# Kernel optimization log

Hardware: AMD Instinct MI355X
Metric: run time of the kernel (lower is better)

Reference implementation:

```python
import jax, jax.numpy as jnp
import numpy as np

NEG = jnp.float32(-1e9)  # -inf surrogate, safe for logsumexp
EPS = 1e-7               # keras.backend.epsilon()


def _ctc_loss(y_true, y_pred):
    """Faithful K.ctc_batch_cost with full input/label lengths.

    y_true: [B, L] int labels in [0, C-2] (blank = C-1, TF convention)
    y_pred: [B, T, C] softmax probabilities
    returns: [B, 1] negative log-likelihood per sample
    """
    B, T, C = y_pred.shape
    L = y_true.shape[1]
    blank = C - 1
    S = 2 * L + 1  # extended label: blank-interleaved

    logp = jnp.log(y_pred + EPS)  # [B, T, C]

    # Extended label sequence [blank, l1, blank, l2, ..., lL, blank]
    ext = jnp.full((B, S), blank, dtype=jnp.int32).at[:, 1::2].set(
        y_true.astype(jnp.int32))  # [B, S]

    # Skip transition (s-2 -> s) allowed iff ext[s] != blank and ext[s] != ext[s-2]
    skip = jnp.concatenate(
        [jnp.zeros((B, 2), dtype=bool),
         (ext[:, 2:] != blank) & (ext[:, 2:] != ext[:, :-2])],
        axis=1)  # [B, S]

    # Gather lattice log-probs once: [B, T, S]
    lp = jnp.take_along_axis(logp, ext[:, None, :], axis=2)

    # alpha at t=0: only states 0 (blank) and 1 (first label) reachable
    alpha0 = jnp.full((B, S), NEG).at[:, 0].set(lp[:, 0, 0]).at[:, 1].set(lp[:, 0, 1])

    def step(alpha, lp_t):
        a1 = alpha                                                     # stay
        a2 = jnp.pad(alpha[:, :-1], ((0, 0), (1, 0)), constant_values=NEG)  # advance 1
        a3 = jnp.pad(alpha[:, :-2], ((0, 0), (2, 0)), constant_values=NEG)  # advance 2
        a3 = jnp.where(skip, a3, NEG)
        new = lp_t + jax.nn.logsumexp(jnp.stack([a1, a2, a3]), axis=0)
        return new, None

    lp_rest = jnp.transpose(lp[:, 1:, :], (1, 0, 2))  # [T-1, B, S]
    alphaT, _ = jax.lax.scan(step, alpha0, lp_rest)

    # Total log-prob ends in last blank or last label
    ll = jax.nn.logsumexp(alphaT[:, S - 2:S], axis=1)  # [B]
    return -ll[:, None]  # [B, 1], matches ctc_batch_cost's expand_dims


def setup_inputs() -> dict:
    key = jax.random.key(0)
    k1, k2 = jax.random.split(key)
    B, T, C, L = 512, 512, 128, 64
    logits = jax.random.normal(k1, (B, T, C), dtype=jnp.float32)
    y_pred = jax.nn.softmax(logits, axis=-1)  # ctc_batch_cost expects probs
    y_true = jax.random.randint(k2, (B, L), 0, C - 1)  # labels exclude blank C-1
    return {"y_true": y_true, "y_pred": y_pred}


def reference(y_true, y_pred):
    return _ctc_loss(y_true, y_pred)
```

## Files before the change

kernel.cpp:

```cpp
#include <hip/hip_runtime.h>


constexpr float EPSF = 1e-7f;
constexpr float LN2F = 0.6931471805599453f;

template<int CTRL>
__device__ __forceinline__ float dpp_mov(float x) {
    return __int_as_float(__builtin_amdgcn_update_dpp(
        0, __float_as_int(x), CTRL, 0xF, 0xF, true));
}

__global__ __launch_bounds__(64)
void ctc_fwd(const int* __restrict__ y_true,
             const float* __restrict__ y_pred,
             float* __restrict__ out)
{
    const int b    = blockIdx.x;
    const int lane = threadIdx.x;

    const float4* __restrict__ gsrc =
        (const float4*)(y_pred + (size_t)b * 512 * 128);

    __shared__ __align__(16) float lds[2 * 2048];

    const int   lab   = y_true[b * 64 + lane];
    const int   labp  = __shfl_up(lab, 1, 64);
    const float skipf = (lane > 0 && lab != labp) ? 1.0f : 0.0f;
    const bool  l0    = (lane == 0);

    float4 regs[3][8];

    auto issueLoads = [&](int chunk, int set) {
        #pragma unroll
        for (int k = 0; k < 8; ++k)
            regs[set][k] = gsrc[chunk * 512 + k * 64 + lane];
    };
    auto writeChunk = [&](int chunk, int set) {
        float* dst = &lds[(chunk & 1) * 2048];
        #pragma unroll
        for (int k = 0; k < 8; ++k)
            *(float4*)(dst + k * 256 + lane * 4) = regs[set][k];
    };

    float plr[4], pbr[4];
    auto issueRead = [&](int t) {
        int tn = t > 511 ? 511 : t;
        const float* rb = &lds[((tn >> 4) & 1) * 2048 + (tn & 15) * 128];
        plr[t & 3] = rb[lab];
        pbr[t & 3] = rb[127];
    };

    float aZ, aA, aB;
    int   shift = 0;
    float red   = 0.0f;

    auto consume = [&](int t, int j) {
        float pl = plr[j & 3] + EPSF;
        float pb = pbr[j & 3] + EPSF;
        float upA = dpp_mov<0x138>(aA);
        float upB = dpp_mov<0x138>(aB);
        upB = l0 ? aZ : upB;
        float ts = fmaf(skipf, upA, aA + upB);
        float nA = pl * ts;
        float nB = pb * (aB + aA);
        aZ *= pb;
        aA = nA; aB = nB;
        if ((j & 7) == 3) {
            float r = fmaxf(fmaxf(aA, aB), aZ);
            r = fmaxf(r, dpp_mov<0x111>(r));
            r = fmaxf(r, dpp_mov<0x112>(r));
            r = fmaxf(r, dpp_mov<0x114>(r));
            r = fmaxf(r, dpp_mov<0x118>(r));
            r = fmaxf(r, dpp_mov<0x142>(r));
            r = fmaxf(r, dpp_mov<0x143>(r));
            red = r;
        }
        if ((j & 7) == 7) {
            int mb = __builtin_amdgcn_readlane(__float_as_int(red), 63);
            int e  = (mb >> 23) & 0xff;
            int f  = 314 - e;
            f = f < 1 ? 1 : (f > 254 ? 254 : f);
            float scale = __int_as_float(f << 23);
            shift += f - 127;
            aA *= scale; aB *= scale; aZ *= scale;
        }
        issueRead(t + 4);
    };

    issueLoads(0, 0); issueLoads(1, 1); issueLoads(2, 2);
    writeChunk(0, 0);
    issueRead(0); issueRead(1); issueRead(2); issueRead(3);
    {
        float pb0 = pbr[0] + EPSF;
        float pl0 = plr[0] + EPSF;
        aZ = pb0;
        aA = l0 ? pl0 : 0.0f;
        aB = 0.0f;
    }
    issueRead(4);

    issueLoads(3, 0);
    writeChunk(1, 1);
    #pragma unroll
    for (int j = 1; j < 16; ++j) consume(j, j);

    for (int cb = 1; cb <= 28; cb += 3) {
        {
            int c = cb;
            if (c + 3 < 32) issueLoads(c + 3, 1);
            writeChunk(c + 1, 2);
            #pragma unroll
            for (int j = 0; j < 16; ++j) consume(16 * c + j, j);
        }
        {
            int c = cb + 1;
            if (c + 3 < 32) issueLoads(c + 3, 2);
            writeChunk(c + 1, 0);
            #pragma unroll
            for (int j = 0; j < 16; ++j) consume(16 * c + j, j);
        }
        {
            int c = cb + 2;
            if (c + 3 < 32) issueLoads(c + 3, 0);
            writeChunk(c + 1, 1);
            #pragma unroll
            for (int j = 0; j < 16; ++j) consume(16 * c + j, j);
        }
    }

    #pragma unroll
    for (int j = 0; j < 16; ++j) consume(16 * 31 + j, j);

    float s   = aA + aB;
    float ll2 = __builtin_amdgcn_logf(s);
    if (lane == 63) out[b] = ((float)shift - ll2) * LN2F;
}

extern "C" void kernel_launch(void* const* d_in, const int* in_sizes, int n_in,
                              void* d_out, int out_size, void* d_ws, size_t ws_size,
                              hipStream_t stream)
{
    const int*   y_true = (const int*)d_in[0];
    const float* y_pred = (const float*)d_in[1];
    float*       out    = (float*)d_out;

    const int B = out_size;
    ctc_fwd<<<dim3(B), dim3(64), 0, stream>>>(y_true, y_pred, out);
}
```

Baseline: 216.8 us.

## Stream probabilities directly into LDS via global_load_lds with 8-deep ring buffer

Replaces the register-staged triple-buffer (global load into VGPRs, then LDS store) with direct global-to-LDS async loads into an 8-chunk ring buffer, throttled by manual vmcnt waits. This is meant to free VGPRs, drop the LDS write instructions from the serial recurrence loop, and keep more loads in flight to hide latency. It raises LDS use to 64KB per block, which may limit occupancy, and correctness depends on the hand-encoded waitcnt values and the absence of barriers within a single wave.

```diff
diff --git a/kernel.cpp b/kernel.cpp
--- a/kernel.cpp
+++ b/kernel.cpp
@@ -10,6 +10,9 @@
         0, __float_as_int(x), CTRL, 0xF, 0xF, true));
 }
 
+#define WAITVM(n) __builtin_amdgcn_s_waitcnt( ((n) & 0xF) | ((((n) >> 4) & 0x3) << 14) \
+                                            | (0x7 << 4) | (0xF << 8) )
+
 __global__ __launch_bounds__(64)
 void ctc_fwd(const int* __restrict__ y_true,
              const float* __restrict__ y_pred,
@@ -18,36 +21,32 @@
     const int b    = blockIdx.x;
     const int lane = threadIdx.x;
 
+    __shared__ __align__(16) float lds[8 * 2048];
+
     const float4* __restrict__ gsrc =
         (const float4*)(y_pred + (size_t)b * 512 * 128);
-
-    __shared__ __align__(16) float lds[2 * 2048];
 
     const int   lab   = y_true[b * 64 + lane];
     const int   labp  = __shfl_up(lab, 1, 64);
     const float skipf = (lane > 0 && lab != labp) ? 1.0f : 0.0f;
     const bool  l0    = (lane == 0);
 
-    float4 regs[3][8];
-
-    auto issueLoads = [&](int chunk, int set) {
+    auto issueChunk = [&](int c) {
+        const float4* g = gsrc + c * 512 + lane;
         #pragma unroll
         for (int k = 0; k < 8; ++k)
-            regs[set][k] = gsrc[chunk * 512 + k * 64 + lane];
-    };
-    auto writeChunk = [&](int chunk, int set) {
-        float* dst = &lds[(chunk & 1) * 2048];
-        #pragma unroll
-        for (int k = 0; k < 8; ++k)
-            *(float4*)(dst + k * 256 + lane * 4) = regs[set][k];
+            __builtin_amdgcn_global_load_lds(
+                (const __attribute__((address_space(1))) void*)(g + k * 64),
+                (__attribute__((address_space(3))) void*)&lds[(c & 7) * 2048 + k * 256],
+                16, 0, 0);
     };
 
     float plr[4], pbr[4];
-    auto issueRead = [&](int t) {
+    auto issueRead = [&](int t, int q) {
         int tn = t > 511 ? 511 : t;
-        const float* rb = &lds[((tn >> 4) & 1) * 2048 + (tn & 15) * 128];
-        plr[t & 3] = rb[lab];
-        pbr[t & 3] = rb[127];
+        const float* rb = &lds[((tn >> 4) & 7) * 2048 + (tn & 15) * 128];
+        plr[q] = rb[lab];
+        pbr[q] = rb[127];
     };
 
     float aZ, aA, aB;
@@ -84,12 +83,12 @@
             shift += f - 127;
             aA *= scale; aB *= scale; aZ *= scale;
         }
-        issueRead(t + 4);
+        issueRead(t + 4, j & 3);
     };
 
-    issueLoads(0, 0); issueLoads(1, 1); issueLoads(2, 2);
-    writeChunk(0, 0);
-    issueRead(0); issueRead(1); issueRead(2); issueRead(3);
+    issueChunk(0); issueChunk(1); issueChunk(2); issueChunk(3);
+    WAITVM(16);
+    issueRead(0, 0); issueRead(1, 1); issueRead(2, 2); issueRead(3, 3);
     {
         float pb0 = pbr[0] + EPSF;
         float pl0 = plr[0] + EPSF;
@@ -97,37 +96,24 @@
         aA = l0 ? pl0 : 0.0f;
         aB = 0.0f;
     }
-    issueRead(4);
+    issueRead(4, 0);
 
-    issueLoads(3, 0);
-    writeChunk(1, 1);
+    issueChunk(4);
     #pragma unroll
     for (int j = 1; j < 16; ++j) consume(j, j);
 
-    for (int cb = 1; cb <= 28; cb += 3) {
-        {
-            int c = cb;
-            if (c + 3 < 32) issueLoads(c + 3, 1);
-            writeChunk(c + 1, 2);
-            #pragma unroll
-            for (int j = 0; j < 16; ++j) consume(16 * c + j, j);
-        }
-        {
-            int c = cb + 1;
-            if (c + 3 < 32) issueLoads(c + 3, 2);
-            writeChunk(c + 1, 0);
-            #pragma unroll
-            for (int j = 0; j < 16; ++j) consume(16 * c + j, j);
-        }
-        {
-            int c = cb + 2;
-            if (c + 3 < 32) issueLoads(c + 3, 0);
-            writeChunk(c + 1, 1);
-            #pragma unroll
-            for (int j = 0; j < 16; ++j) consume(16 * c + j, j);
-        }
+    for (int c = 1; c <= 28; ++c) {
+        WAITVM(16);
+        if (c <= 27) issueChunk(c + 4);
+        #pragma unroll
+        for (int j = 0; j < 16; ++j) consume(16 * c + j, j);
     }
-
+    WAITVM(8);
+    #pragma unroll
+    for (int j = 0; j < 16; ++j) consume(16 * 29 + j, j);
+    WAITVM(0);
+    #pragma unroll
+    for (int j = 0; j < 16; ++j) consume(16 * 30 + j, j);
     #pragma unroll
     for (int j = 0; j < 16; ++j) consume(16 * 31 + j, j);
 
```

Result: faster. 192.0 us (-11.4%).
